# Performance work log

Hardware: AMD Instinct MI355X
Metric: run time of the kernel (lower is better)

The kernel has to match this reference:

```python
import math
import jax, jax.numpy as jnp
import numpy as np

N_HEAD = 16

def setup_inputs() -> dict:
    key = jax.random.key(0)
    ks = jax.random.split(key, 3)
    B, T, C = 2, 2048, 1024
    x = jax.random.normal(ks[0], (B, T, C), dtype=jnp.float32)
    W_kqv = jax.random.normal(ks[1], (3 * C, C), dtype=jnp.float32) * 0.02
    b_kqv = jnp.zeros((3 * C,), dtype=jnp.float32)
    W_proj = jax.random.normal(ks[2], (C, C), dtype=jnp.float32) * 0.02
    b_proj = jnp.zeros((C,), dtype=jnp.float32)
    return {"x": x, "W_kqv": W_kqv, "b_kqv": b_kqv, "W_proj": W_proj, "b_proj": b_proj}

def reference(x, W_kqv, b_kqv, W_proj, b_proj):
    B, T, C = x.shape
    nh = N_HEAD
    hd = C // nh
    # fused QKV projection, then view [B,T,nh,3*hd] and slice into k,q,v
    kqv = (x @ W_kqv.T + b_kqv).reshape(B, T, nh, 3, hd)
    k = kqv[..., 0, :]  # [B,T,nh,hd]
    q = kqv[..., 1, :]
    v = kqv[..., 2, :]
    scale = 1.0 / math.sqrt(hd)
    att = jnp.einsum("bthd,bshd->bhts", q, k) * scale  # [B,nh,T,T]
    causal = jnp.tril(jnp.ones((T, T), dtype=bool))
    att = jnp.where(causal[None, None], att, -jnp.inf)
    att = jax.nn.softmax(att, axis=-1)
    y = jnp.einsum("bhts,bshd->bthd", att, v).reshape(B, T, C)
    return y @ W_proj.T + b_proj
```

## Files before the change

### kernel.cpp

```cpp
#include <hip/hip_runtime.h>

#define TSEQ 2048
#define NHEAD 16
#define HD 64
#define CDIM 1024
#define BT 4096

typedef unsigned short u16;
typedef __bf16 bf16x8 __attribute__((ext_vector_type(8)));
typedef float f32x4 __attribute__((ext_vector_type(4)));
typedef float f32x16 __attribute__((ext_vector_type(16)));

union Frag {
  int4 i4;
  bf16x8 b;
  u16 u[8];
};

__device__ __forceinline__ u16 f2b(float f) {
  union { float f; unsigned u; } x;
  x.f = f;
  unsigned r = x.u + 0x7fffu + ((x.u >> 16) & 1u);
  return (u16)(r >> 16);
}

#define N4X 1048576
#define N4W1 786432
#define N4W2 262144
__global__ void cvt3_kernel(const float* __restrict__ x, const float* __restrict__ w1,
                            const float* __restrict__ w2, u16* __restrict__ ox,
                            u16* __restrict__ o1, u16* __restrict__ o2) {
  int i = blockIdx.x * blockDim.x + threadIdx.x;
  int stride = gridDim.x * blockDim.x;
  for (int idx = i; idx < N4X + N4W1 + N4W2; idx += stride) {
    const float4* src;
    ushort4* dst;
    int k;
    if (idx < N4X) { src = (const float4*)x; dst = (ushort4*)ox; k = idx; }
    else if (idx < N4X + N4W1) { src = (const float4*)w1; dst = (ushort4*)o1; k = idx - N4X; }
    else { src = (const float4*)w2; dst = (ushort4*)o2; k = idx - N4X - N4W1; }
    float4 f = src[k];
    ushort4 o;
    o.x = f2b(f.x); o.y = f2b(f.y); o.z = f2b(f.z); o.w = f2b(f.w);
    dst[k] = o;
  }
}

__device__ __forceinline__ void gload_lds16(const u16* g, u16* l) {
  __builtin_amdgcn_global_load_lds((__attribute__((address_space(1))) void*)g,
                                   (__attribute__((address_space(3))) void*)l, 16, 0, 0);
}

__device__ __forceinline__ void gemm_tiles(const u16* __restrict__ A, const u16* __restrict__ Bw,
                                           int K, int m0, int n0,
                                           u16 (*__restrict__ Ash)[128 * 32],
                                           u16 (*__restrict__ Bsh)[128 * 32],
                                           f32x4 acc[4][4]) {
  const int tid = threadIdx.x;
  const int lane = tid & 63;
  const int w = tid >> 6;
  const int wr = (w >> 1) * 64, wc = (w & 1) * 64;
  const int lr = lane & 15;
  const int hi = lane >> 4;
  const int r0 = tid >> 2;
  const int cS = ((tid & 3) ^ ((tid >> 3) & 3)) << 3;
  const int frg = (hi ^ ((lr >> 1) & 3)) << 3;

#define GSTAGE(B, KO)                                                                 \
  { _Pragma("unroll") for (int s = 0; s < 2; s++) {                                   \
      gload_lds16(&A[(size_t)(m0 + s * 64 + r0) * K + (KO) + cS], &Ash[B][(s * 256 + tid) * 8]); \
      gload_lds16(&Bw[(size_t)(n0 + s * 64 + r0) * K + (KO) + cS], &Bsh[B][(s * 256 + tid) * 8]); \
  } }

  GSTAGE(0, 0)
  int cur = 0;
  for (int k0 = 0; k0 < K; k0 += 32) {
    __syncthreads();
    Frag af[4], bfr[4];
#pragma unroll
    for (int i = 0; i < 4; i++) {
      af[i].i4 = *(const int4*)&Ash[cur][(wr + i * 16 + lr) * 32 + frg];
      bfr[i].i4 = *(const int4*)&Bsh[cur][(wc + i * 16 + lr) * 32 + frg];
    }
    __builtin_amdgcn_sched_barrier(0);
    if (k0 + 32 < K) GSTAGE(cur ^ 1, k0 + 32)
    __builtin_amdgcn_sched_barrier(0);
#pragma unroll
    for (int mf = 0; mf < 4; mf++)
#pragma unroll
      for (int nf = 0; nf < 4; nf++)
        acc[mf][nf] = __builtin_amdgcn_mfma_f32_16x16x32_bf16(af[mf].b, bfr[nf].b, acc[mf][nf], 0, 0, 0);
    cur ^= 1;
  }
#undef GSTAGE
}

__global__ __launch_bounds__(256) void gemm_kqv(const u16* __restrict__ xb, const u16* __restrict__ wb,
                                                const float* __restrict__ bias,
                                                u16* __restrict__ qb, u16* __restrict__ kb,
                                                u16* __restrict__ vtb) {
  __shared__ __align__(16) u16 SMEMU[16384];
  u16 (*Ash)[4096] = (u16(*)[4096])&SMEMU[0];
  u16 (*Bsh)[4096] = (u16(*)[4096])&SMEMU[8192];
  const int m0 = blockIdx.y * 128, n0 = blockIdx.x * 128;
  f32x4 acc[4][4];
#pragma unroll
  for (int i = 0; i < 4; i++)
#pragma unroll
    for (int j = 0; j < 4; j++) acc[i][j] = (f32x4){0.f, 0.f, 0.f, 0.f};

  gemm_tiles(xb, wb, CDIM, m0, n0, Ash, Bsh, acc);

  const int tid = threadIdx.x;
  const int lane = tid & 63;
  const int w = tid >> 6;
  const int wr = (w >> 1) * 64, wc = (w & 1) * 64;
  const int lr = lane & 15;
  const int rbase = (lane >> 4) << 2;

  __syncthreads();
  u16* Csh = SMEMU;
#pragma unroll
  for (int mf = 0; mf < 4; mf++) {
#pragma unroll
    for (int nf = 0; nf < 4; nf++) {
      f32x4 a = acc[mf][nf];
      int nl = wc + nf * 16 + lr;
      int n = n0 + nl;
      float bval = bias[n];
      int sres = ((n0 + wc + nf * 16) % 192) >> 6;
      float scale = (sres == 1) ? 0.125f : 1.f;
#pragma unroll
      for (int r = 0; r < 4; r++) {
        int ml = wr + mf * 16 + rbase + r;
        Csh[ml * 128 + (nl ^ (((ml >> 2) & 3) << 4))] = f2b((a[r] + bval) * scale);
      }
    }
  }
  __syncthreads();

  const int bb = m0 >> 11, tt = m0 & 2047;
#pragma unroll
  for (int j = 0; j < 2; j++) {
    int ns = n0 + j * 64;
    int h = ns / 192;
    int sres = (ns % 192) >> 6;
    int bh2 = (bb << 4) + h;
    if (sres == 2) {
      int ch = tid & 15;
      int d0 = tid >> 4;
#pragma unroll
      for (int it = 0; it < 4; it++) {
        int d = d0 + it * 16;
        unsigned pk[4];
#pragma unroll
        for (int p = 0; p < 4; p++) {
          int c0 = ch * 8 + p * 2;
          int g0 = c0 >> 6, c6a = c0 & 63;
          int mA = g0 * 64 + ((c6a & 51) | ((c6a & 8) >> 1) | ((c6a & 4) << 1));
          int c1 = c0 + 1;
          int g1 = c1 >> 6, c6b = c1 & 63;
          int mB = g1 * 64 + ((c6b & 51) | ((c6b & 8) >> 1) | ((c6b & 4) << 1));
          unsigned lo = Csh[mA * 128 + ((j * 64 + d) ^ (((mA >> 2) & 3) << 4))];
          unsigned hi2 = Csh[mB * 128 + ((j * 64 + d) ^ (((mB >> 2) & 3) << 4))];
          pk[p] = lo | (hi2 << 16);
        }
        int4 v4; v4.x = pk[0]; v4.y = pk[1]; v4.z = pk[2]; v4.w = pk[3];
        *(int4*)&vtb[((size_t)bh2 * HD + d) * TSEQ + tt + ch * 8] = v4;
      }
    } else {
      u16* dst = (sres == 0) ? kb : qb;
      int ch = tid & 7;
      int rg = tid >> 3;
#pragma unroll
      for (int it = 0; it < 4; it++) {
        int m = rg + it * 32;
        int ccp = (j * 8 + ch) ^ (((m >> 2) & 3) << 1);
        int4 v4 = *(const int4*)&Csh[m * 128 + (ccp << 3)];
        *(int4*)&dst[((size_t)bh2 * TSEQ + tt + m) * HD + ch * 8] = v4;
      }
    }
  }
}

__device__ __forceinline__ void gemm_tiles64(const u16* __restrict__ A, const u16* __restrict__ Bw,
                                             int K, int m0, int n0,
                                             u16 (*__restrict__ Ash)[2048],
                                             u16 (*__restrict__ Bsh)[4096],
                                             f32x4 acc[2][4]) {
  const int tid = threadIdx.x;
  const int lane = tid & 63;
  const int w = tid >> 6;
  const int wr = (w >> 1) * 32, wc = (w & 1) * 64;
  const int lr = lane & 15;
  const int hi = lane >> 4;
  const int r0 = tid >> 2;
  const int cS = ((tid & 3) ^ ((tid >> 3) & 3)) << 3;
  const int frg = (hi ^ ((lr >> 1) & 3)) << 3;

#define GSTAGE64(B, KO)                                                               \
  {                                                                                   \
    gload_lds16(&A[(size_t)(m0 + r0) * K + (KO) + cS], &Ash[B][tid * 8]);             \
    _Pragma("unroll") for (int s = 0; s < 2; s++)                                     \
      gload_lds16(&Bw[(size_t)(n0 + s * 64 + r0) * K + (KO) + cS], &Bsh[B][(s * 256 + tid) * 8]); \
  }

  GSTAGE64(0, 0)
  int cur = 0;
  for (int k0 = 0; k0 < K; k0 += 32) {
    __syncthreads();
    Frag af[2], bfr[4];
#pragma unroll
    for (int i = 0; i < 2; i++)
      af[i].i4 = *(const int4*)&Ash[cur][(wr + i * 16 + lr) * 32 + frg];
#pragma unroll
    for (int i = 0; i < 4; i++)
      bfr[i].i4 = *(const int4*)&Bsh[cur][(wc + i * 16 + lr) * 32 + frg];
    __builtin_amdgcn_sched_barrier(0);
    if (k0 + 32 < K) GSTAGE64(cur ^ 1, k0 + 32)
    __builtin_amdgcn_sched_barrier(0);
#pragma unroll
    for (int mf = 0; mf < 2; mf++)
#pragma unroll
      for (int nf = 0; nf < 4; nf++)
        acc[mf][nf] = __builtin_amdgcn_mfma_f32_16x16x32_bf16(af[mf].b, bfr[nf].b, acc[mf][nf], 0, 0, 0);
    cur ^= 1;
  }
#undef GSTAGE64
}

__global__ __launch_bounds__(256) void gemm_proj(const u16* __restrict__ yb, const u16* __restrict__ wb,
                                                 const float* __restrict__ bias,
                                                 float* __restrict__ out) {
  __shared__ __align__(16) u16 Ash[2][2048];
  __shared__ __align__(16) u16 Bsh[2][4096];
  const int m0 = blockIdx.y * 64, n0 = blockIdx.x * 128;
  f32x4 acc[2][4];
#pragma unroll
  for (int i = 0; i < 2; i++)
#pragma unroll
    for (int j = 0; j < 4; j++) acc[i][j] = (f32x4){0.f, 0.f, 0.f, 0.f};

  gemm_tiles64(yb, wb, CDIM, m0, n0, Ash, Bsh, acc);

  const int tid = threadIdx.x;
  const int lane = tid & 63;
  const int w = tid >> 6;
  const int wr = (w >> 1) * 32, wc = (w & 1) * 64;
  const int lr = lane & 15;
  const int rbase = (lane >> 4) << 2;
#pragma unroll
  for (int mf = 0; mf < 2; mf++) {
#pragma unroll
    for (int nf = 0; nf < 4; nf++) {
      f32x4 a = acc[mf][nf];
      int n = n0 + wc + nf * 16 + lr;
      float bval = bias[n];
#pragma unroll
      for (int r = 0; r < 4; r++) {
        int m = m0 + wr + mf * 16 + rbase + r;
        out[(size_t)m * CDIM + n] = a[r] + bval;
      }
    }
  }
}

__global__ __launch_bounds__(256, 2) void attn_kernel(const u16* __restrict__ qb,
                                                      const u16* __restrict__ kb,
                                                      const u16* __restrict__ vtb,
                                                      u16* __restrict__ yb) {
  __shared__ u16 Ksh[2][64 * 64];
  __shared__ u16 Vsh[2][64 * 64];

  const int tid = threadIdx.x;
  const int lane = tid & 63;
  const int w = tid >> 6;
  const int l31 = lane & 31;
  const int hi32 = lane >> 5;
  const int swz = l31 & 7;

  const int jj = blockIdx.x;
  const int bh = jj & 31;
  const int cls = jj >> 5;
  const int qbk = (cls < 8) ? (15 - cls) : (cls - 8);
  const int q0w = qbk * 128 + w * 32;
  const int LN = 2 * qbk + 2;
  const int jd = q0w >> 6;
  const int qg = q0w + l31;

  const u16* Qp = qb + (size_t)bh * TSEQ * HD;
  const u16* Kp = kb + (size_t)bh * TSEQ * HD;
  const u16* Vt = vtb + (size_t)bh * HD * TSEQ;

  Frag qf[4];
#pragma unroll
  for (int k = 0; k < 4; k++)
    qf[k].i4 = *(const int4*)&Qp[(size_t)(q0w + l31) * HD + k * 16 + hi32 * 8];

  f32x16 O0, O1;
  float lp = 0.f;
#pragma unroll
  for (int i = 0; i < 16; i++) { O0[i] = 0.f; O1[i] = 0.f; }

#define STAGE(B, JT)                                                                 \
  {                                                                                  \
    const int kvb = (JT) * 64;                                                       \
    _Pragma("unroll") for (int p = 0; p < 2; p++) {                                  \
      int c = tid + p * 256;                                                         \
      int row = c >> 3, c16 = c & 7;                                                 \
      int gofs = (c16 ^ (row & 7)) << 3;                                             \
      gload_lds16(&Kp[(size_t)(kvb + row) * HD + gofs], &Ksh[B][c * 8]);             \
      gload_lds16(&Vt[(size_t)row * TSEQ + kvb + gofs], &Vsh[B][c * 8]);             \
    }                                                                                \
  }

#define PACK2(dst, SV, base)                                                         \
    asm("v_cvt_pk_bf16_f32 %0, %1, %2" : "=v"(dst.i4.x) : "v"(SV[base + 0]), "v"(SV[base + 1])); \
    asm("v_cvt_pk_bf16_f32 %0, %1, %2" : "=v"(dst.i4.y) : "v"(SV[base + 2]), "v"(SV[base + 3])); \
    asm("v_cvt_pk_bf16_f32 %0, %1, %2" : "=v"(dst.i4.z) : "v"(SV[base + 4]), "v"(SV[base + 5])); \
    asm("v_cvt_pk_bf16_f32 %0, %1, %2" : "=v"(dst.i4.w) : "v"(SV[base + 6]), "v"(SV[base + 7]));

  STAGE(0, 0)
  int cur = 0;
  for (int jt = 0; jt < LN; ++jt) {
    __syncthreads();
    const int kv0 = jt * 64;
    const bool act = (jt <= jd);
    const bool run1 = (kv0 + 32) <= (q0w + 31);

    Frag ka0[4], ka1[4], vf0[4], vf1[4];
    if (act) {
      const u16* Kt = Ksh[cur];
      const u16* Vl = Vsh[cur];
#pragma unroll
      for (int k = 0; k < 4; k++) {
        int ch = ((2 * k + hi32) ^ swz) << 3;
        ka0[k].i4 = *(const int4*)&Kt[l31 * 64 + ch];
        vf0[k].i4 = *(const int4*)&Vl[l31 * 64 + ch];
        vf1[k].i4 = *(const int4*)&Vl[(32 + l31) * 64 + ch];
      }
      if (run1) {
#pragma unroll
        for (int k = 0; k < 4; k++) {
          int ch = ((2 * k + hi32) ^ swz) << 3;
          ka1[k].i4 = *(const int4*)&Kt[(32 + l31) * 64 + ch];
        }
      }
    }
    __builtin_amdgcn_sched_barrier(0);
    if (jt + 1 < LN) STAGE(cur ^ 1, jt + 1)
    __builtin_amdgcn_sched_barrier(0);
    if (act) {
      const bool diag = (jt == jd);
      f32x16 S;
#pragma unroll
      for (int i = 0; i < 16; i++) S[i] = 0.f;
      __builtin_amdgcn_s_setprio(1);
#pragma unroll
      for (int k = 0; k < 4; k++)
        S = __builtin_amdgcn_mfma_f32_32x32x16_bf16(ka0[k].b, qf[k].b, S, 0, 0, 0);
      __builtin_amdgcn_s_setprio(0);
      if (diag) {
#pragma unroll
        for (int reg = 0; reg < 16; reg++) {
          int crow = (reg & 3) + 8 * (reg >> 2) + 4 * hi32;
          S[reg] = (kv0 + crow <= qg) ? __expf(S[reg]) : 0.f;
        }
      } else {
#pragma unroll
        for (int reg = 0; reg < 16; reg++) S[reg] = __expf(S[reg]);
      }
#pragma unroll
      for (int reg = 0; reg < 16; reg++) lp += S[reg];
      Frag pa[2];
      PACK2(pa[0], S, 0)
      PACK2(pa[1], S, 8)
      __builtin_amdgcn_s_setprio(1);
#pragma unroll
      for (int k = 0; k < 2; k++) {
        O0 = __builtin_amdgcn_mfma_f32_32x32x16_bf16(pa[k].b, vf0[k].b, O0, 0, 0, 0);
        O1 = __builtin_amdgcn_mfma_f32_32x32x16_bf16(pa[k].b, vf1[k].b, O1, 0, 0, 0);
      }
      __builtin_amdgcn_s_setprio(0);
      if (run1) {
        f32x16 T;
#pragma unroll
        for (int i = 0; i < 16; i++) T[i] = 0.f;
        __builtin_amdgcn_s_setprio(1);
#pragma unroll
        for (int k = 0; k < 4; k++)
          T = __builtin_amdgcn_mfma_f32_32x32x16_bf16(ka1[k].b, qf[k].b, T, 0, 0, 0);
        __builtin_amdgcn_s_setprio(0);
        if (diag) {
#pragma unroll
          for (int reg = 0; reg < 16; reg++) {
            int crow = (reg & 3) + 8 * (reg >> 2) + 4 * hi32;
            T[reg] = (kv0 + 32 + crow <= qg) ? __expf(T[reg]) : 0.f;
          }
        } else {
#pragma unroll
          for (int reg = 0; reg < 16; reg++) T[reg] = __expf(T[reg]);
        }
#pragma unroll
        for (int reg = 0; reg < 16; reg++) lp += T[reg];
        Frag pb[2];
        PACK2(pb[0], T, 0)
        PACK2(pb[1], T, 8)
        __builtin_amdgcn_s_setprio(1);
#pragma unroll
        for (int k = 0; k < 2; k++) {
          O0 = __builtin_amdgcn_mfma_f32_32x32x16_bf16(pb[k].b, vf0[k + 2].b, O0, 0, 0, 0);
          O1 = __builtin_amdgcn_mfma_f32_32x32x16_bf16(pb[k].b, vf1[k + 2].b, O1, 0, 0, 0);
        }
        __builtin_amdgcn_s_setprio(0);
      }
    }
    cur ^= 1;
  }
#undef STAGE
#undef PACK2

  float lpt = lp + __shfl_xor(lp, 32);
  const int b = bh >> 4, h = bh & 15;
#pragma unroll
  for (int reg = 0; reg < 16; reg++) {
    int qlocal = (reg & 3) + 8 * (reg >> 2) + 4 * hi32;
    float invr = 1.f / __shfl(lpt, qlocal);
    int t = q0w + qlocal;
    size_t rowoff = ((size_t)(b * TSEQ + t) << 10) + (h << 6);
    yb[rowoff + l31] = f2b(O0[reg] * invr);
    yb[rowoff + 32 + l31] = f2b(O1[reg] * invr);
  }
}

extern "C" void kernel_launch(void* const* d_in, const int* in_sizes, int n_in,
                              void* d_out, int out_size, void* d_ws, size_t ws_size,
                              hipStream_t stream) {
  const float* x = (const float*)d_in[0];
  const float* Wkqv = (const float*)d_in[1];
  const float* bkqv = (const float*)d_in[2];
  const float* Wproj = (const float*)d_in[3];
  const float* bproj = (const float*)d_in[4];
  float* out = (float*)d_out;

  u16* ws = (u16*)d_ws;
  u16* xb = ws;
  u16* wkqvb = xb + 4194304;
  u16* wprojb = wkqvb + 3145728;
  u16* qb = wprojb + 1048576;
  u16* kb = qb + 4194304;
  u16* vtb = kb + 4194304;
  u16* yb = vtb + 4194304;

  cvt3_kernel<<<2048, 256, 0, stream>>>(x, Wkqv, Wproj, xb, wkqvb, wprojb);
  gemm_kqv<<<dim3(24, 32), 256, 0, stream>>>(xb, wkqvb, bkqv, qb, kb, vtb);
  attn_kernel<<<512, 256, 0, stream>>>(qb, kb, vtb, yb);
  gemm_proj<<<dim3(8, 64), 256, 0, stream>>>(yb, wprojb, bproj, out);
}
```

Measured before the change: 96.00 us.

## Widen attention KV tile to 128 keys per stage

The attention loop now stages 128 keys of K and V per iteration instead of 64. This halves the number of barrier-synchronized iterations, and each warp handles four 32-key sub-tiles, with causal masking applied only on the final diagonal tile. The V layout in LDS becomes 64x128 with a new swizzle. This is meant to cut barrier and loop overhead, but it doubles LDS use and raises register pressure from holding 4x4 K fragments plus V fragments, which could reduce occupancy under launch_bounds(256,2).

Measured after the change: 94.23 us. No clear change (-1.8%).

```diff
diff --git a/kernel.cpp b/kernel.cpp
--- a/kernel.cpp
+++ b/kernel.cpp
@@ -269,8 +269,8 @@
                                                       const u16* __restrict__ kb,
                                                       const u16* __restrict__ vtb,
                                                       u16* __restrict__ yb) {
-  __shared__ u16 Ksh[2][64 * 64];
-  __shared__ u16 Vsh[2][64 * 64];
+  __shared__ u16 Ksh[2][128 * 64];
+  __shared__ u16 Vsh[2][64 * 128];
 
   const int tid = threadIdx.x;
   const int lane = tid & 63;
@@ -284,9 +284,7 @@
   const int cls = jj >> 5;
   const int qbk = (cls < 8) ? (15 - cls) : (cls - 8);
   const int q0w = qbk * 128 + w * 32;
-  const int LN = 2 * qbk + 2;
-  const int jd = q0w >> 6;
-  const int qg = q0w + l31;
+  const int LN = qbk + 1;
 
   const u16* Qp = qb + (size_t)bh * TSEQ * HD;
   const u16* Kp = kb + (size_t)bh * TSEQ * HD;
@@ -304,12 +302,17 @@
 
 #define STAGE(B, JT)                                                                 \
   {                                                                                  \
-    const int kvb = (JT) * 64;                                                       \
-    _Pragma("unroll") for (int p = 0; p < 2; p++) {                                  \
+    const int kvb = (JT) * 128;                                                      \
+    _Pragma("unroll") for (int p = 0; p < 4; p++) {                                  \
       int c = tid + p * 256;                                                         \
       int row = c >> 3, c16 = c & 7;                                                 \
-      int gofs = (c16 ^ (row & 7)) << 3;                                             \
-      gload_lds16(&Kp[(size_t)(kvb + row) * HD + gofs], &Ksh[B][c * 8]);             \
+      gload_lds16(&Kp[(size_t)(kvb + row) * HD + ((c16 ^ (row & 7)) << 3)],          \
+                  &Ksh[B][c * 8]);                                                   \
+    }                                                                                \
+    _Pragma("unroll") for (int p = 0; p < 4; p++) {                                  \
+      int c = tid + p * 256;                                                         \
+      int row = c >> 4, c16 = c & 15;                                                \
+      int gofs = ((c16 >> 3) << 6) + (((c16 & 7) ^ (row & 7)) << 3);                 \
       gload_lds16(&Vt[(size_t)row * TSEQ + kvb + gofs], &Vsh[B][c * 8]);             \
     }                                                                                \
   }
@@ -324,93 +327,60 @@
   int cur = 0;
   for (int jt = 0; jt < LN; ++jt) {
     __syncthreads();
-    const int kv0 = jt * 64;
-    const bool act = (jt <= jd);
-    const bool run1 = (kv0 + 32) <= (q0w + 31);
-
-    Frag ka0[4], ka1[4], vf0[4], vf1[4];
-    if (act) {
-      const u16* Kt = Ksh[cur];
-      const u16* Vl = Vsh[cur];
-#pragma unroll
-      for (int k = 0; k < 4; k++) {
-        int ch = ((2 * k + hi32) ^ swz) << 3;
-        ka0[k].i4 = *(const int4*)&Kt[l31 * 64 + ch];
-        vf0[k].i4 = *(const int4*)&Vl[l31 * 64 + ch];
-        vf1[k].i4 = *(const int4*)&Vl[(32 + l31) * 64 + ch];
-      }
-      if (run1) {
-#pragma unroll
-        for (int k = 0; k < 4; k++) {
-          int ch = ((2 * k + hi32) ^ swz) << 3;
-          ka1[k].i4 = *(const int4*)&Kt[(32 + l31) * 64 + ch];
+    const bool diag = (jt == LN - 1);
+    const int wlim = diag ? w : 3;
+    const u16* Kt = Ksh[cur];
+    const u16* Vl = Vsh[cur];
+
+    Frag ka[4][4], vA[4][2], vB[4][2];
+#pragma unroll
+    for (int sh = 0; sh < 4; ++sh) {
+      if (sh <= wlim) {
+#pragma unroll
+        for (int k = 0; k < 4; ++k)
+          ka[sh][k].i4 = *(const int4*)&Kt[(sh * 32 + l31) * 64 + (((2 * k + hi32) ^ swz) << 3)];
+#pragma unroll
+        for (int k = 0; k < 2; ++k) {
+          int cofs = ((sh >> 1) << 6) + (((((sh & 1) << 2) + 2 * k + hi32) ^ swz) << 3);
+          vA[sh][k].i4 = *(const int4*)&Vl[l31 * 128 + cofs];
+          vB[sh][k].i4 = *(const int4*)&Vl[(32 + l31) * 128 + cofs];
         }
       }
     }
     __builtin_amdgcn_sched_barrier(0);
     if (jt + 1 < LN) STAGE(cur ^ 1, jt + 1)
     __builtin_amdgcn_sched_barrier(0);
-    if (act) {
-      const bool diag = (jt == jd);
-      f32x16 S;
-#pragma unroll
-      for (int i = 0; i < 16; i++) S[i] = 0.f;
-      __builtin_amdgcn_s_setprio(1);
-#pragma unroll
-      for (int k = 0; k < 4; k++)
-        S = __builtin_amdgcn_mfma_f32_32x32x16_bf16(ka0[k].b, qf[k].b, S, 0, 0, 0);
-      __builtin_amdgcn_s_setprio(0);
-      if (diag) {
-#pragma unroll
-        for (int reg = 0; reg < 16; reg++) {
-          int crow = (reg & 3) + 8 * (reg >> 2) + 4 * hi32;
-          S[reg] = (kv0 + crow <= qg) ? __expf(S[reg]) : 0.f;
-        }
-      } else {
-#pragma unroll
-        for (int reg = 0; reg < 16; reg++) S[reg] = __expf(S[reg]);
-      }
-#pragma unroll
-      for (int reg = 0; reg < 16; reg++) lp += S[reg];
-      Frag pa[2];
-      PACK2(pa[0], S, 0)
-      PACK2(pa[1], S, 8)
-      __builtin_amdgcn_s_setprio(1);
-#pragma unroll
-      for (int k = 0; k < 2; k++) {
-        O0 = __builtin_amdgcn_mfma_f32_32x32x16_bf16(pa[k].b, vf0[k].b, O0, 0, 0, 0);
-        O1 = __builtin_amdgcn_mfma_f32_32x32x16_bf16(pa[k].b, vf1[k].b, O1, 0, 0, 0);
-      }
-      __builtin_amdgcn_s_setprio(0);
-      if (run1) {
-        f32x16 T;
-#pragma unroll
-        for (int i = 0; i < 16; i++) T[i] = 0.f;
+#pragma unroll
+    for (int sh = 0; sh < 4; ++sh) {
+      if (sh <= wlim) {
+        f32x16 S;
+#pragma unroll
+        for (int i = 0; i < 16; i++) S[i] = 0.f;
         __builtin_amdgcn_s_setprio(1);
 #pragma unroll
         for (int k = 0; k < 4; k++)
-          T = __builtin_amdgcn_mfma_f32_32x32x16_bf16(ka1[k].b, qf[k].b, T, 0, 0, 0);
+          S = __builtin_amdgcn_mfma_f32_32x32x16_bf16(ka[sh][k].b, qf[k].b, S, 0, 0, 0);
         __builtin_amdgcn_s_setprio(0);
-        if (diag) {
+        if (diag && sh == w) {
 #pragma unroll
           for (int reg = 0; reg < 16; reg++) {
             int crow = (reg & 3) + 8 * (reg >> 2) + 4 * hi32;
-            T[reg] = (kv0 + 32 + crow <= qg) ? __expf(T[reg]) : 0.f;
+            S[reg] = (crow <= l31) ? __expf(S[reg]) : 0.f;
           }
         } else {
 #pragma unroll
-          for (int reg = 0; reg < 16; reg++) T[reg] = __expf(T[reg]);
+          for (int reg = 0; reg < 16; reg++) S[reg] = __expf(S[reg]);
         }
 #pragma unroll
-        for (int reg = 0; reg < 16; reg++) lp += T[reg];
-        Frag pb[2];
-        PACK2(pb[0], T, 0)
-        PACK2(pb[1], T, 8)
+        for (int reg = 0; reg < 16; reg++) lp += S[reg];
+        Frag pa[2];
+        PACK2(pa[0], S, 0)
+        PACK2(pa[1], S, 8)
         __builtin_amdgcn_s_setprio(1);
 #pragma unroll
         for (int k = 0; k < 2; k++) {
-          O0 = __builtin_amdgcn_mfma_f32_32x32x16_bf16(pb[k].b, vf0[k + 2].b, O0, 0, 0, 0);
-          O1 = __builtin_amdgcn_mfma_f32_32x32x16_bf16(pb[k].b, vf1[k + 2].b, O1, 0, 0, 0);
+          O0 = __builtin_amdgcn_mfma_f32_32x32x16_bf16(pa[k].b, vA[sh][k].b, O0, 0, 0, 0);
+          O1 = __builtin_amdgcn_mfma_f32_32x32x16_bf16(pa[k].b, vB[sh][k].b, O1, 0, 0, 0);
         }
         __builtin_amdgcn_s_setprio(0);
       }
```
